# Optimization experiments

Hardware: AMD Instinct MI355X
Metric: run time of the kernel (lower is better)

The kernel has to match this reference:

```python
import jax, jax.numpy as jnp
import numpy as np

L, E, H, R = 6, 1024, 8, 33
DH = E // H
FF = 4 * E
B, S = 8, 512


def _layer_norm(x, g, b, eps=1e-5):
    m = jnp.mean(x, axis=-1, keepdims=True)
    v = jnp.mean(jnp.square(x - m), axis=-1, keepdims=True)
    return (x - m) * jax.lax.rsqrt(v + eps) * g + b


def setup_inputs() -> dict:
    key = jax.random.key(0)
    ks = jax.random.split(key, 24)
    rn = lambda k, shape, s=0.02: (jax.random.normal(k, shape, jnp.float32) * s)
    inp = {
        'enc_padded': jax.random.normal(ks[0], (B, S, E), jnp.float32),
        'relations': jax.random.randint(ks[1], (B, S, S), 0, R),
        'enc_lengths': jax.random.randint(ks[2], (B,), 1, S + 1),
        'Wq': rn(ks[3], (L, E, E)), 'bq': jnp.zeros((L, E), jnp.float32),
        'Wk': rn(ks[4], (L, E, E)), 'bk': jnp.zeros((L, E), jnp.float32),
        'Wv': rn(ks[5], (L, E, E)), 'bv': jnp.zeros((L, E), jnp.float32),
        'Wo': rn(ks[6], (L, E, E)), 'bo': jnp.zeros((L, E), jnp.float32),
        'rel_k': rn(ks[7], (L, R, DH)),
        'rel_v': rn(ks[8], (L, R, DH)),
        'W1': rn(ks[9], (L, E, FF)), 'b1': jnp.zeros((L, FF), jnp.float32),
        'W2': rn(ks[10], (L, FF, E)), 'b2': jnp.zeros((L, E), jnp.float32),
        'ln1_g': jnp.ones((L, E), jnp.float32), 'ln1_b': jnp.zeros((L, E), jnp.float32),
        'ln2_g': jnp.ones((L, E), jnp.float32), 'ln2_b': jnp.zeros((L, E), jnp.float32),
        'lnf_g': jnp.ones((E,), jnp.float32), 'lnf_b': jnp.zeros((E,), jnp.float32),
    }
    return inp


def reference(enc_padded, relations, enc_lengths, Wq, bq, Wk, bk, Wv, bv, Wo, bo,
              rel_k, rel_v, W1, b1, W2, b2, ln1_g, ln1_b, ln2_g, ln2_b, lnf_g, lnf_b):
    x = enc_padded  # [B,S,E]
    dt = x.dtype
    # attention mask: valid iff both query and key positions are within seq length
    pos = jnp.arange(S)
    valid = pos[None, :] < enc_lengths[:, None]            # [B,S]
    mask2d = valid[:, :, None] & valid[:, None, :]          # [B,S,S]
    # one-hot relation indicator, shared across layers (R=33 is small)
    rel_oh = jax.nn.one_hot(relations, R, dtype=dt)        # [B,S,S,R]
    scale = 1.0 / np.sqrt(DH).astype(np.float32)

    def split_heads(t):  # [B,S,E] -> [B,H,S,DH]
        return t.reshape(B, S, H, DH).transpose(0, 2, 1, 3)

    for l in range(L):
        # --- relation-aware self-attention (pre-LN sublayer) ---
        h = _layer_norm(x, ln1_g[l], ln1_b[l])
        q = split_heads(h @ Wq[l] + bq[l])
        k = split_heads(h @ Wk[l] + bk[l])
        v = split_heads(h @ Wv[l] + bv[l])
        scores = jnp.einsum('bhid,bhjd->bhij', q, k)
        # relation key bias: q_i . rel_k[rel[i,j]]  via small [B,H,S,R] GEMM + one-hot contraction
        qr = jnp.einsum('bhid,rd->bhir', q, rel_k[l])
        scores = (scores + jnp.einsum('bhir,bijr->bhij', qr, rel_oh)) * scale
        scores = jnp.where(mask2d[:, None], scores, jnp.asarray(-1e9, dt))
        attn = jax.nn.softmax(scores, axis=-1)              # [B,H,S,S]
        out = jnp.einsum('bhij,bhjd->bhid', attn, v)
        # relation value bias: sum_j attn_ij * rel_v[rel[i,j]]
        a_rel = jnp.einsum('bhij,bijr->bhir', attn, rel_oh)
        out = out + jnp.einsum('bhir,rd->bhid', a_rel, rel_v[l])
        out = out.transpose(0, 2, 1, 3).reshape(B, S, E) @ Wo[l] + bo[l]
        x = x + out
        # --- position-wise feed-forward (pre-LN sublayer) ---
        h2 = _layer_norm(x, ln2_g[l], ln2_b[l])
        x = x + (jax.nn.relu(h2 @ W1[l] + b1[l]) @ W2[l] + b2[l])
    return _layer_norm(x, lnf_g, lnf_b)
```

## Files before the change

### kernel.cpp

```cpp
#include <hip/hip_runtime.h>

#define LNUM 6
#define EDIM 1024
#define HNUM 8
#define DHD  128
#define RNUM 33
#define FFD  4096
#define BNUM 8
#define SLEN 512
#define TOK  (BNUM*SLEN)

typedef __attribute__((ext_vector_type(8))) short bf16x8;
typedef __attribute__((ext_vector_type(4))) float f32x4;
typedef unsigned short u16;
typedef unsigned int u32;

__device__ __forceinline__ u16 f2b(float f) {
  u32 u = __builtin_bit_cast(u32, f);
  u32 r = u + 0x7FFFu + ((u >> 16) & 1u);
  return (u16)(r >> 16);
}
__device__ __forceinline__ u32 pck(float a, float b) { return (u32)f2b(a) | ((u32)f2b(b) << 16); }

#define GL16(gp, lp) __builtin_amdgcn_global_load_lds(                        \
    (const __attribute__((address_space(1))) void*)(gp),                      \
    (__attribute__((address_space(3))) void*)(lp), 16, 0, 0)

#define WAITVM20 do { asm volatile("s_waitcnt vmcnt(20)" ::: "memory"); \
                      __builtin_amdgcn_sched_barrier(0); } while (0)
#define WAITVM16 do { asm volatile("s_waitcnt vmcnt(16)" ::: "memory"); \
                      __builtin_amdgcn_sched_barrier(0); } while (0)
#define WAITVM8 do { asm volatile("s_waitcnt vmcnt(8)" ::: "memory"); \
                     __builtin_amdgcn_sched_barrier(0); } while (0)
#define WAITVM0 do { asm volatile("s_waitcnt vmcnt(0)" ::: "memory"); \
                     __builtin_amdgcn_sched_barrier(0); } while (0)

template<int BF16OUT>
__global__ __launch_bounds__(256) void ln_kernel(const float* __restrict__ x,
                                                 const float* __restrict__ g,
                                                 const float* __restrict__ be,
                                                 void* __restrict__ o) {
  int row = blockIdx.x;
  int t = threadIdx.x;
  const float* xr = x + (size_t)row * EDIM;
  float4 xv = *reinterpret_cast<const float4*>(xr + t * 4);
  float s1 = xv.x + xv.y + xv.z + xv.w;
  float s2 = xv.x*xv.x + xv.y*xv.y + xv.z*xv.z + xv.w*xv.w;
#pragma unroll
  for (int off = 32; off >= 1; off >>= 1) {
    s1 += __shfl_down(s1, off, 64);
    s2 += __shfl_down(s2, off, 64);
  }
  __shared__ float r1[4], r2[4];
  if ((t & 63) == 0) { r1[t >> 6] = s1; r2[t >> 6] = s2; }
  __syncthreads();
  s1 = r1[0] + r1[1] + r1[2] + r1[3];
  s2 = r2[0] + r2[1] + r2[2] + r2[3];
  float mean = s1 * (1.0f / EDIM);
  float var  = s2 * (1.0f / EDIM) - mean * mean;
  float rstd = rsqrtf(var + 1e-5f);
  float4 gv = *reinterpret_cast<const float4*>(g + t * 4);
  float4 bv = *reinterpret_cast<const float4*>(be + t * 4);
  float o0 = (xv.x - mean) * rstd * gv.x + bv.x;
  float o1 = (xv.y - mean) * rstd * gv.y + bv.y;
  float o2 = (xv.z - mean) * rstd * gv.z + bv.z;
  float o3 = (xv.w - mean) * rstd * gv.w + bv.w;
  if (BF16OUT) {
    ushort4 ov; ov.x = f2b(o0); ov.y = f2b(o1); ov.z = f2b(o2); ov.w = f2b(o3);
    *reinterpret_cast<ushort4*>((u16*)o + (size_t)row * EDIM + t * 4) = ov;
  } else {
    *reinterpret_cast<float4*>((float*)o + (size_t)row * EDIM + t * 4) = make_float4(o0, o1, o2, o3);
  }
}

__global__ __launch_bounds__(256) void wtrans(const float* __restrict__ src0,
                                              u16* __restrict__ dst0,
                                              int Kd, int Nd, size_t sstride, size_t dstride) {
  __shared__ float Ts[32][33];
  const float* src = src0 + blockIdx.z * sstride;
  u16* dst = dst0 + blockIdx.z * dstride;
  int r0 = blockIdx.y * 32, c0 = blockIdx.x * 32;
  int ty = threadIdx.x >> 3, tx = threadIdx.x & 7;
  float4 v = *reinterpret_cast<const float4*>(src + (size_t)(r0 + ty) * Nd + c0 + tx * 4);
  Ts[ty][tx*4+0] = v.x; Ts[ty][tx*4+1] = v.y; Ts[ty][tx*4+2] = v.z; Ts[ty][tx*4+3] = v.w;
  __syncthreads();
  ushort4 o;
  o.x = f2b(Ts[tx*4+0][ty]); o.y = f2b(Ts[tx*4+1][ty]);
  o.z = f2b(Ts[tx*4+2][ty]); o.w = f2b(Ts[tx*4+3][ty]);
  *reinterpret_cast<ushort4*>(dst + (size_t)(c0 + ty) * Kd + r0 + tx * 4) = o;
}

__global__ __launch_bounds__(256) void relpack(const int* __restrict__ rel,
                                               unsigned char* __restrict__ out) {
  __shared__ int Ts[32][33];
  int bz = blockIdx.z;
  int r0 = blockIdx.y * 32, c0 = blockIdx.x * 32;
  int ty = threadIdx.x >> 3, tx = threadIdx.x & 7;
  const int* src = rel + (size_t)bz * SLEN * SLEN;
  int4 v = *reinterpret_cast<const int4*>(src + (size_t)(r0 + ty) * SLEN + c0 + tx * 4);
  Ts[ty][tx*4+0] = v.x; Ts[ty][tx*4+1] = v.y; Ts[ty][tx*4+2] = v.z; Ts[ty][tx*4+3] = v.w;
  __syncthreads();
  u32 o = (u32)(Ts[tx*4+0][ty] & 255) | ((u32)(Ts[tx*4+1][ty] & 255) << 8) |
          ((u32)(Ts[tx*4+2][ty] & 255) << 16) | ((u32)(Ts[tx*4+3][ty] & 255) << 24);
  *reinterpret_cast<u32*>(out + (size_t)bz * SLEN * SLEN + (size_t)(c0 + ty) * SLEN + r0 + tx * 4) = o;
}

template<int DEPTH, int BIASMODE, int ACT, int RES, int OUTBF16>
__global__ __launch_bounds__(256) void gemm_bt(const u16* __restrict__ A,
                                               const u16* __restrict__ B,
                                               const float* __restrict__ bias0,
                                               const float* __restrict__ bias1,
                                               const float* __restrict__ res,
                                               void* __restrict__ Cv,
                                               int M, int N, int K) {
  __shared__ u16 As[DEPTH][128 * 64];
  __shared__ u16 Bs[DEPTH][128 * 64];
  int t = threadIdx.x;
  int l = t & 63, w = t >> 6;
  int wm = w & 1, wn = w >> 1;
  int m0 = blockIdx.y * 128, n0 = blockIdx.x * 128;
  f32x4 acc[4][4] = {};
  const u16* Agp = A + (size_t)(m0 + w * 32 + (l >> 3)) * K + (l & 7) * 8;
  const u16* Bgp = B + (size_t)(n0 + w * 32 + (l >> 3)) * K + (l & 7) * 8;
  const int nst = K >> 6;
  auto issue = [&](int k0, int bi) {
#pragma unroll
    for (int u = 0; u < 4; ++u) {
      GL16(Agp + (size_t)(u * 8) * K + k0, &As[bi][w * 2048 + u * 512]);
      GL16(Bgp + (size_t)(u * 8) * K + k0, &Bs[bi][w * 2048 + u * 512]);
    }
  };
  issue(0, 0);
  if (DEPTH == 3 && nst > 1) issue(64, 1);
  for (int i = 0; i < nst; ++i) {
    int cur = (DEPTH == 3) ? (i % 3) : (i & 1);
    if (DEPTH == 3) {
      if (i + 2 < nst)      { issue((i + 2) * 64, (i + 2) % 3); WAITVM16; }
      else if (i + 1 < nst) { WAITVM8; }
      else                  { WAITVM0; }
    } else {
      if (i + 1 < nst) { issue((i + 1) * 64, cur ^ 1); WAITVM8; }
      else             { WAITVM0; }
    }
    __builtin_amdgcn_s_barrier();
    const u16* Asc = As[cur];
    const u16* Bsc = Bs[cur];
#pragma unroll
    for (int d4 = 0; d4 < 2; ++d4) {
      bf16x8 af[4];
#pragma unroll
      for (int fm = 0; fm < 4; ++fm) {
        int row = wm * 64 + fm * 16 + (l & 15);
        af[fm] = *reinterpret_cast<const bf16x8*>(Asc + row * 64 + (d4 * 4 + (l >> 4)) * 8);
      }
#pragma unroll
      for (int fn = 0; fn < 4; ++fn) {
        int row = wn * 64 + fn * 16 + (l & 15);
        bf16x8 bf = *reinterpret_cast<const bf16x8*>(Bsc + row * 64 + (d4 * 4 + (l >> 4)) * 8);
#pragma unroll
        for (int fm = 0; fm < 4; ++fm)
          acc[fm][fn] = __builtin_amdgcn_mfma_f32_16x16x32_bf16(af[fm], bf, acc[fm][fn], 0, 0, 0);
      }
    }
    __builtin_amdgcn_s_barrier();
  }
#pragma unroll
  for (int fm = 0; fm < 4; ++fm)
#pragma unroll
    for (int fn = 0; fn < 4; ++fn)
#pragma unroll
      for (int e = 0; e < 4; ++e) {
        int m = m0 + wm * 64 + fm * 16 + (l >> 4) * 4 + e;
        int n = n0 + wn * 64 + fn * 16 + (l & 15);
        float v = acc[fm][fn][e];
        if (BIASMODE == 0) v += bias0[n];
        if (BIASMODE == 1) v += bias0[m];
        if (BIASMODE == 2) v += (n < 1024) ? bias0[n] : bias1[n - 1024];
        if (ACT == 1) v = fmaxf(v, 0.f);
        if (RES == 1) v += res[(size_t)m * N + n];
        if (OUTBF16) ((u16*)Cv)[(size_t)m * N + n] = f2b(v);
        else ((float*)Cv)[(size_t)m * N + n] = v;
      }
}

template<int BIASMODE, int ACT, int RES, int OUTBF16>
__global__ __launch_bounds__(512, 2) void gemm_big(const u16* __restrict__ A,
                                                   const u16* __restrict__ B,
                                                   const float* __restrict__ bias0,
                                                   const float* __restrict__ res,
                                                   void* __restrict__ Cv,
                                                   int M, int N, int K) {
  __shared__ u16 As[2][256 * 64];
  __shared__ u16 Bs[2][256 * 64];
  int t = threadIdx.x;
  int l = t & 63, w = t >> 6;
  int wm = w >> 2, wn = w & 3;
  int m0 = blockIdx.y * 256, n0 = blockIdx.x * 256;
  f32x4 acc[8][4] = {};
  const u16* Agp = A + (size_t)(m0 + w * 32 + (l >> 3)) * K + (l & 7) * 8;
  const u16* Bgp = B + (size_t)(n0 + w * 32 + (l >> 3)) * K + (l & 7) * 8;
  const int nst = K >> 6;
  auto issue = [&](int k0, int bi) {
#pragma unroll
    for (int u = 0; u < 4; ++u) {
      GL16(Agp + (size_t)(u * 8) * K + k0, &As[bi][w * 2048 + u * 512]);
      GL16(Bgp + (size_t)(u * 8) * K + k0, &Bs[bi][w * 2048 + u * 512]);
    }
  };
  issue(0, 0);
  for (int i = 0; i < nst; ++i) {
    int cur = i & 1;
    if (i + 1 < nst) { issue((i + 1) * 64, cur ^ 1); WAITVM8; }
    else             { WAITVM0; }
    __builtin_amdgcn_s_barrier();
    const u16* Asc = As[cur];
    const u16* Bsc = Bs[cur];
#pragma unroll
    for (int d4 = 0; d4 < 2; ++d4) {
      bf16x8 bf[4];
#pragma unroll
      for (int fn = 0; fn < 4; ++fn) {
        int row = wn * 64 + fn * 16 + (l & 15);
        bf[fn] = *reinterpret_cast<const bf16x8*>(Bsc + row * 64 + (d4 * 4 + (l >> 4)) * 8);
      }
#pragma unroll
      for (int fm = 0; fm < 8; ++fm) {
        int row = wm * 128 + fm * 16 + (l & 15);
        bf16x8 af = *reinterpret_cast<const bf16x8*>(Asc + row * 64 + (d4 * 4 + (l >> 4)) * 8);
#pragma unroll
        for (int fn = 0; fn < 4; ++fn)
          acc[fm][fn] = __builtin_amdgcn_mfma_f32_16x16x32_bf16(af, bf[fn], acc[fm][fn], 0, 0, 0);
      }
    }
    __builtin_amdgcn_s_barrier();
  }
#pragma unroll
  for (int fm = 0; fm < 8; ++fm)
#pragma unroll
    for (int fn = 0; fn < 4; ++fn)
#pragma unroll
      for (int e = 0; e < 4; ++e) {
        int m = m0 + wm * 128 + fm * 16 + (l >> 4) * 4 + e;
        int n = n0 + wn * 64 + fn * 16 + (l & 15);
        float v = acc[fm][fn][e];
        if (BIASMODE == 0) v += bias0[n];
        if (ACT == 1) v = fmaxf(v, 0.f);
        if (RES == 1) v += res[(size_t)m * N + n];
        if (OUTBF16) ((u16*)Cv)[(size_t)m * N + n] = f2b(v);
        else ((float*)Cv)[(size_t)m * N + n] = v;
      }
}

#define A_P  0
#define A_Q  16384
#define A_PS 32768
#define A_QR 40960
#define A_AR 50176
#define A_LS 59392
#define A_SM 59648

__global__ __launch_bounds__(256, 2) void attn_kernel(const u16* __restrict__ qk,
                                                      const u16* __restrict__ vt,
                                                      const unsigned char* __restrict__ rel8,
                                                      const int* __restrict__ lens,
                                                      const float* __restrict__ relk,
                                                      const float* __restrict__ relv,
                                                      u16* __restrict__ outb) {
  __align__(16) __shared__ char sm[A_SM];
  char*  Pb  = sm + A_P;
  char*  Qb  = sm + A_Q;
  char*  PSb = sm + A_PS;
  float* QR  = (float*)(sm + A_QR);
  float* AREL = (float*)(sm + A_AR);
  float* LSUM = (float*)(sm + A_LS);

  const int t = threadIdx.x;
  const int l = t & 63, w = t >> 6;
  const int lg = l >> 4;
  const int ll = l & 15;
  const int bx = blockIdx.x;
  const int xcd = bx & 7, rem = bx >> 3, slot = rem & 7, it = rem >> 3;
  const int g = slot * 8 + xcd;
  const int b = g >> 3, hh = g & 7;
  const int i0 = it * 64;
  const int len = lens[b];
  const float scale = 0.08838834764831845f;
  char* PSw = PSb + w * 2048;

  auto issueK = [&](int kt) {
#pragma unroll
    for (int u = 0; u < 4; ++u) {
      int row = w * 16 + u * 4 + (lg);
      int sb = (ll * 16) ^ (((u * 4 + lg) & 7) << 4);
      const u16* gp = qk + (size_t)(b * SLEN + kt * 64 + row) * 2048 + 1024 + hh * DHD + (sb >> 1);
      GL16(gp, Pb + (w * 4 + u) * 1024);
    }
  };
  auto issueV = [&](int kt) {
#pragma unroll
    for (int u = 0; u < 4; ++u) {
      int row = w * 32 + u * 8 + (l >> 3);
      int sb = ((l & 7) * 16) ^ ((l >> 3) << 4);
      const u16* gp = vt + (size_t)(hh * DHD + row) * TOK + b * SLEN + kt * 64 + (sb >> 1);
      GL16(gp, Qb + (w * 4 + u) * 1024);
    }
  };
  const unsigned char* relbase = rel8 + (size_t)b * SLEN * SLEN + (i0 + w * 16 + lg * 4);

  for (int idx = l; idx < 16 * 36; idx += 64) AREL[w * 16 * 36 + idx] = 0.f;
  if (t < 192) {
    int r = t >> 2, sub = t & 3;
#pragma unroll
    for (int u = 0; u < 4; ++u) {
      int seg = sub * 4 + u;
      uint4 o;
      if (r < RNUM) {
        float4 f0 = *reinterpret_cast<const float4*>(relk + r * DHD + seg * 8);
        float4 f1 = *reinterpret_cast<const float4*>(relk + r * DHD + seg * 8 + 4);
        o.x = pck(f0.x, f0.y); o.y = pck(f0.z, f0.w);
        o.z = pck(f1.x, f1.y); o.w = pck(f1.z, f1.w);
      } else { o.x = o.y = o.z = o.w = 0u; }
      *reinterpret_cast<uint4*>(Pb + r * 256 + ((seg * 16) ^ ((r & 7) << 4))) = o;
    }
  }
  bf16x8 aq[4];
  {
    const u16* qrow = qk + (size_t)(b * SLEN + i0 + w * 16 + ll) * 2048 + hh * DHD;
#pragma unroll
    for (int d4 = 0; d4 < 4; ++d4)
      aq[d4] = *reinterpret_cast<const bf16x8*>(qrow + (d4 * 4 + lg) * 8);
  }
  __syncthreads();
#pragma unroll
  for (int rb = 0; rb < 3; ++rb) {
    f32x4 acc = {};
#pragma unroll
    for (int d4 = 0; d4 < 4; ++d4) {
      int rr = rb * 16 + ll;
      bf16x8 br = *reinterpret_cast<const bf16x8*>(Pb + rr * 256 + (((d4 * 4 + lg) * 16) ^ ((rr & 7) << 4)));
      acc = __builtin_amdgcn_mfma_f32_16x16x32_bf16(aq[d4], br, acc, 0, 0, 0);
    }
    int col = rb * 16 + ll;
    if (col < 36)
#pragma unroll
      for (int e = 0; e < 4; ++e)
        QR[(w * 16 + lg * 4 + e) * 36 + col] = acc[e];
  }
  __syncthreads();
  issueK(0);
  u32 relw[4];
  {
    const unsigned char* rb = relbase + (size_t)ll * SLEN;
#pragma unroll
    for (int fj = 0; fj < 4; ++fj)
      relw[fj] = *reinterpret_cast<const u32*>(rb + (size_t)(fj * 16) * SLEN);
  }

  bool rowv[4];
#pragma unroll
  for (int e = 0; e < 4; ++e) rowv[e] = (i0 + w * 16 + lg * 4 + e) < len;

  float m_[4];
#pragma unroll
  for (int e = 0; e < 4; ++e) m_[e] = -3.0e38f;
  f32x4 oacc[8] = {};

  for (int kt = 0; kt < 8; ++kt) {
    issueV(kt);
    WAITVM20;
    __builtin_amdgcn_s_barrier();
    __builtin_amdgcn_s_setprio(1);
    f32x4 sacc[4];
#pragma unroll
    for (int fj = 0; fj < 4; ++fj) {
      f32x4 a = {};
#pragma unroll
      for (int d4 = 0; d4 < 4; ++d4) {
        int row = fj * 16 + ll;
        bf16x8 bk_ = *reinterpret_cast<const bf16x8*>(Pb + row * 256 + (((d4 * 4 + lg) * 16) ^ ((row & 7) << 4)));
        a = __builtin_amdgcn_mfma_f32_16x16x32_bf16(aq[d4], bk_, a, 0, 0, 0);
      }
      sacc[fj] = a;
    }
    __builtin_amdgcn_s_setprio(0);
#pragma unroll
    for (int fj = 0; fj < 4; ++fj) {
      bool colv = (kt * 64 + fj * 16 + ll) < len;
      u32 rw = relw[fj];
#pragma unroll
      for (int e = 0; e < 4; ++e) {
        int r = (rw >> (8 * e)) & 255;
        float s = (sacc[fj][e] + QR[(w * 16 + lg * 4 + e) * 36 + r]) * scale;
        s = (rowv[e] && colv) ? s : -1e9f;
        sacc[fj][e] = s;
      }
    }
    float pl[4];
#pragma unroll
    for (int e = 0; e < 4; ++e)
      pl[e] = fmaxf(fmaxf(sacc[0][e], sacc[1][e]), fmaxf(sacc[2][e], sacc[3][e]));
    bool ok = (pl[0] <= m_[0] + 8.f) && (pl[1] <= m_[1] + 8.f) &&
              (pl[2] <= m_[2] + 8.f) && (pl[3] <= m_[3] + 8.f);
    if (!__all(ok)) {
#pragma unroll
      for (int e = 0; e < 4; ++e) {
        float px = pl[e];
        px = fmaxf(px, __shfl_xor(px, 1, 64));
        px = fmaxf(px, __shfl_xor(px, 2, 64));
        px = fmaxf(px, __shfl_xor(px, 4, 64));
        px = fmaxf(px, __shfl_xor(px, 8, 64));
        float mn = fmaxf(m_[e], px);
        float f = __expf(m_[e] - mn);
        m_[e] = mn;
#pragma unroll
        for (int fd = 0; fd < 8; ++fd) oacc[fd][e] *= f;
        if (f != 1.0f) {
          int row = w * 16 + lg * 4 + e;
          AREL[row * 36 + ll] *= f;
          AREL[row * 36 + 16 + ll] *= f;
          if (ll == 0) AREL[row * 36 + 32] *= f;
        }
      }
    }
#pragma unroll
    for (int fj = 0; fj < 4; ++fj) {
      u32 rw = relw[fj];
#pragma unroll
      for (int e = 0; e < 4; ++e) {
        float p = __expf(sacc[fj][e] - m_[e]);
        int iloc = lg * 4 + e;
        atomicAdd(&AREL[(w * 16 + iloc) * 36 + ((rw >> (8 * e)) & 255)], p);
        *reinterpret_cast<u16*>(PSw + iloc * 128 + (((fj * 16 + ll) * 2) ^ ((iloc & 7) << 4))) = f2b(p);
      }
    }
    __builtin_amdgcn_s_barrier();
    if (kt < 7) {
      issueK(kt + 1);
      {
        const unsigned char* rb = relbase + (size_t)((kt + 1) * 64 + ll) * SLEN;
#pragma unroll
        for (int fj = 0; fj < 4; ++fj)
          relw[fj] = *reinterpret_cast<const u32*>(rb + (size_t)(fj * 16) * SLEN);
      }
      WAITVM20;
    } else {
      WAITVM0;
    }
    __builtin_amdgcn_s_barrier();
    __builtin_amdgcn_s_setprio(1);
#pragma unroll
    for (int kc = 0; kc < 2; ++kc) {
      bf16x8 pa = *reinterpret_cast<const bf16x8*>(PSw + ll * 128 + (((kc * 4 + lg) * 16) ^ ((ll & 7) << 4)));
#pragma unroll
      for (int fd = 0; fd < 8; ++fd) {
        int row = fd * 16 + ll;
        bf16x8 vb = *reinterpret_cast<const bf16x8*>(Qb + row * 128 + (((kc * 4 + lg) * 16) ^ ((row & 7) << 4)));
        oacc[fd] = __builtin_amdgcn_mfma_f32_16x16x32_bf16(pa, vb, oacc[fd], 0, 0, 0);
      }
    }
    __builtin_amdgcn_s_setprio(0);
    __builtin_amdgcn_s_barrier();
  }
  if (l < 16) {
    int row = w * 16 + l;
    float s = 0.f;
    for (int r = 0; r < RNUM; ++r) s += AREL[row * 36 + r];
    LSUM[row] = s;
  }
#pragma unroll
  for (int e = 0; e < 4; ++e) {
    float inv = 1.0f / LSUM[w * 16 + lg * 4 + e];
#pragma unroll
    for (int fd = 0; fd < 8; ++fd) oacc[fd][e] *= inv;
  }
  for (int idx = t; idx < 128 * 64; idx += 256) {
    int d = idx >> 6, r = idx & 63;
    u16 v = (r < RNUM) ? f2b(relv[r * DHD + d]) : (u16)0;
    *reinterpret_cast<u16*>(Pb + d * 128 + ((r * 2) ^ ((d & 7) << 4))) = v;
  }
  for (int idx = l; idx < 1024; idx += 64) {
    int ri = idx >> 6, r = idx & 63;
    int row = w * 16 + ri;
    float v = (r < RNUM) ? AREL[row * 36 + r] * (1.0f / LSUM[row]) : 0.f;
    *reinterpret_cast<u16*>(PSw + ri * 128 + ((r * 2) ^ ((ri & 7) << 4))) = f2b(v);
  }
  __syncthreads();
#pragma unroll
  for (int kc = 0; kc < 2; ++kc) {
    bf16x8 pa = *reinterpret_cast<const bf16x8*>(PSw + ll * 128 + (((kc * 4 + lg) * 16) ^ ((ll & 7) << 4)));
#pragma unroll
    for (int fd = 0; fd < 8; ++fd) {
      int row = fd * 16 + ll;
      bf16x8 vb = *reinterpret_cast<const bf16x8*>(Pb + row * 128 + (((kc * 4 + lg) * 16) ^ ((row & 7) << 4)));
      oacc[fd] = __builtin_amdgcn_mfma_f32_16x16x32_bf16(pa, vb, oacc[fd], 0, 0, 0);
    }
  }
  char* OSw = Qb + w * 4096;
#pragma unroll
  for (int fd = 0; fd < 8; ++fd)
#pragma unroll
    for (int e = 0; e < 4; ++e)
      *reinterpret_cast<u16*>(OSw + ((lg * 4 + e) * 128 + fd * 16 + ll) * 2) = f2b(oacc[fd][e]);
  __syncthreads();
  {
    int ri = l >> 2, q4 = l & 3;
    const char* srcb = OSw + ri * 256 + q4 * 64;
    u16* dst = outb + (size_t)(b * SLEN + i0 + w * 16 + ri) * EDIM + hh * DHD + q4 * 32;
    uint4 x0 = *reinterpret_cast<const uint4*>(srcb);
    uint4 x1 = *reinterpret_cast<const uint4*>(srcb + 16);
    uint4 x2 = *reinterpret_cast<const uint4*>(srcb + 32);
    uint4 x3 = *reinterpret_cast<const uint4*>(srcb + 48);
    *reinterpret_cast<uint4*>(dst)      = x0;
    *reinterpret_cast<uint4*>(dst + 8)  = x1;
    *reinterpret_cast<uint4*>(dst + 16) = x2;
    *reinterpret_cast<uint4*>(dst + 24) = x3;
  }
}

extern "C" void kernel_launch(void* const* d_in, const int* in_sizes, int n_in,
                              void* d_out, int out_size, void* d_ws, size_t ws_size,
                              hipStream_t stream) {
  const float* enc  = (const float*)d_in[0];
  const int*   rel  = (const int*)d_in[1];
  const int*   lens = (const int*)d_in[2];
  const float* Wq = (const float*)d_in[3];
  const float* bq = (const float*)d_in[4];
  const float* Wk = (const float*)d_in[5];
  const float* bk = (const float*)d_in[6];
  const float* Wv = (const float*)d_in[7];
  const float* bv = (const float*)d_in[8];
  const float* Wo = (const float*)d_in[9];
  const float* bo = (const float*)d_in[10];
  const float* relk = (const float*)d_in[11];
  const float* relv = (const float*)d_in[12];
  const float* W1 = (const float*)d_in[13];
  const float* b1 = (const float*)d_in[14];
  const float* W2 = (const float*)d_in[15];
  const float* b2 = (const float*)d_in[16];
  const float* ln1g = (const float*)d_in[17];
  const float* ln1b = (const float*)d_in[18];
  const float* ln2g = (const float*)d_in[19];
  const float* ln2b = (const float*)d_in[20];
  const float* lnfg = (const float*)d_in[21];
  const float* lnfb = (const float*)d_in[22];
  float* out = (float*)d_out;

  char* W = (char*)d_ws;
  u16* h     = (u16*)W;
  unsigned char* rel8_h = (unsigned char*)W;
  char* U    = W + 8388608;
  u16* qkb   = (u16*)U;
  u16* vtb   = (u16*)(U + 16777216);
  u16* attno = (u16*)(U + 25165824);
  u16* mid   = (u16*)U;
  bool xin = ws_size >= (size_t)83886080;
  float* x = xin ? (float*)(W + 41943040) : out;
  size_t wt_off = xin ? 58720256 : 41943040;
  char* WT = W + wt_off;
  bool big = ws_size >= (size_t)209715200;

  const size_t EE = (size_t)EDIM * EDIM;
  const size_t EF = (size_t)EDIM * FFD;
  size_t wt_bytes = (big ? 6 : 1) * (size_t)(2*EE + EE + EE + EF + EF) * 2;
  bool rel_ded = ws_size >= wt_off + wt_bytes + (size_t)BNUM * SLEN * SLEN + 256;
  unsigned char* rel8 = rel_ded ? (unsigned char*)(WT + wt_bytes) : rel8_h;

  u16 *WqkT, *WvT, *WoT, *W1T, *W2T;
  dim3 blk(256);
  if (big) {
    u16* wqk_all = (u16*)WT;
    u16* wv_all  = wqk_all + 6 * 2 * EE;
    u16* wo_all  = wv_all + 6 * EE;
    u16* w1_all  = wo_all + 6 * EE;
    u16* w2_all  = w1_all + 6 * EF;
    wtrans<<<dim3(32, 32, 6), blk, 0, stream>>>(Wq, wqk_all, 1024, 1024, EE, 2 * EE);
    wtrans<<<dim3(32, 32, 6), blk, 0, stream>>>(Wk, wqk_all + EE, 1024, 1024, EE, 2 * EE);
    wtrans<<<dim3(32, 32, 6), blk, 0, stream>>>(Wv, wv_all, 1024, 1024, EE, EE);
    wtrans<<<dim3(32, 32, 6), blk, 0, stream>>>(Wo, wo_all, 1024, 1024, EE, EE);
    wtrans<<<dim3(128, 32, 6), blk, 0, stream>>>(W1, w1_all, 1024, 4096, EF, EF);
    wtrans<<<dim3(32, 128, 6), blk, 0, stream>>>(W2, w2_all, 4096, 1024, EF, EF);
    WqkT = wqk_all; WvT = wv_all; WoT = wo_all; W1T = w1_all; W2T = w2_all;
  } else {
    WqkT = (u16*)WT;
    WvT  = WqkT + 2 * EE;
    WoT  = WvT + EE;
    W1T  = WoT + EE;
    W2T  = W1T + EF;
  }
  if (rel_ded) relpack<<<dim3(16, 16, 8), blk, 0, stream>>>(rel, rel8);

  dim3 gLN(TOK);
  for (int ll = 0; ll < LNUM; ++ll) {
    u16 *wqkT, *wvT, *woT, *w1T, *w2T;
    if (big) {
      wqkT = WqkT + (size_t)ll * 2 * EE; wvT = WvT + (size_t)ll * EE; woT = WoT + (size_t)ll * EE;
      w1T = W1T + (size_t)ll * EF; w2T = W2T + (size_t)ll * EF;
    } else {
      wqkT = WqkT; wvT = WvT; woT = WoT; w1T = W1T; w2T = W2T;
      wtrans<<<dim3(32, 32, 1), blk, 0, stream>>>(Wq + ll * EE, wqkT, 1024, 1024, 0, 0);
      wtrans<<<dim3(32, 32, 1), blk, 0, stream>>>(Wk + ll * EE, wqkT + EE, 1024, 1024, 0, 0);
      wtrans<<<dim3(32, 32, 1), blk, 0, stream>>>(Wv + ll * EE, wvT, 1024, 1024, 0, 0);
      wtrans<<<dim3(32, 32, 1), blk, 0, stream>>>(Wo + ll * EE, woT, 1024, 1024, 0, 0);
      wtrans<<<dim3(128, 32, 1), blk, 0, stream>>>(W1 + ll * EF, w1T, 1024, 4096, 0, 0);
      wtrans<<<dim3(32, 128, 1), blk, 0, stream>>>(W2 + ll * EF, w2T, 4096, 1024, 0, 0);
    }
    const float* xin_p = (ll == 0) ? enc : x;
    ln_kernel<1><<<gLN, blk, 0, stream>>>(xin_p, ln1g + ll * EDIM, ln1b + ll * EDIM, h);
    gemm_bt<2, 2, 0, 0, 1><<<dim3(16, 32), blk, 0, stream>>>(h, wqkT, bq + ll * EDIM, bk + ll * EDIM,
                                                             nullptr, qkb, TOK, 2048, EDIM);
    gemm_bt<3, 1, 0, 0, 1><<<dim3(32, 8), blk, 0, stream>>>(wvT, h, bv + ll * EDIM, nullptr,
                                                            nullptr, vtb, EDIM, TOK, EDIM);
    if (!rel_ded) relpack<<<dim3(16, 16, 8), blk, 0, stream>>>(rel, rel8);
    attn_kernel<<<dim3(512), blk, 0, stream>>>(qkb, vtb, rel8, lens,
                                               relk + (size_t)ll * RNUM * DHD,
                                               relv + (size_t)ll * RNUM * DHD, attno);
    gemm_bt<3, 0, 0, 1, 0><<<dim3(8, 32), blk, 0, stream>>>(attno, woT, bo + ll * EDIM, nullptr,
                                                            xin_p, x, TOK, EDIM, EDIM);
    ln_kernel<1><<<gLN, blk, 0, stream>>>(x, ln2g + ll * EDIM, ln2b + ll * EDIM, h);
    gemm_big<0, 1, 0, 1><<<dim3(FFD / 256, TOK / 256), dim3(512), 0, stream>>>(
        h, w1T, b1 + ll * FFD, nullptr, mid, TOK, FFD, EDIM);
    gemm_bt<3, 0, 0, 1, 0><<<dim3(8, 32), blk, 0, stream>>>(mid, w2T, b2 + ll * EDIM, nullptr,
                                                            x, x, TOK, EDIM, FFD);
  }
  ln_kernel<0><<<gLN, blk, 0, stream>>>(x, lnfg, lnfb, out);
}
```

Before: 2.158 ms.

## Halve attention KV tile and shrink LDS to fit four blocks per CU

```diff
diff --git a/kernel.cpp b/kernel.cpp
--- a/kernel.cpp
+++ b/kernel.cpp
@@ -20,17 +20,20 @@
   u32 r = u + 0x7FFFu + ((u >> 16) & 1u);
   return (u16)(r >> 16);
 }
+__device__ __forceinline__ float b2f(u16 v) {
+  return __builtin_bit_cast(float, ((u32)v) << 16);
+}
 __device__ __forceinline__ u32 pck(float a, float b) { return (u32)f2b(a) | ((u32)f2b(b) << 16); }
 
 #define GL16(gp, lp) __builtin_amdgcn_global_load_lds(                        \
     (const __attribute__((address_space(1))) void*)(gp),                      \
     (__attribute__((address_space(3))) void*)(lp), 16, 0, 0)
 
-#define WAITVM20 do { asm volatile("s_waitcnt vmcnt(20)" ::: "memory"); \
-                      __builtin_amdgcn_sched_barrier(0); } while (0)
 #define WAITVM16 do { asm volatile("s_waitcnt vmcnt(16)" ::: "memory"); \
                       __builtin_amdgcn_sched_barrier(0); } while (0)
 #define WAITVM8 do { asm volatile("s_waitcnt vmcnt(8)" ::: "memory"); \
+                     __builtin_amdgcn_sched_barrier(0); } while (0)
+#define WAITVM4 do { asm volatile("s_waitcnt vmcnt(4)" ::: "memory"); \
                      __builtin_amdgcn_sched_barrier(0); } while (0)
 #define WAITVM0 do { asm volatile("s_waitcnt vmcnt(0)" ::: "memory"); \
                      __builtin_amdgcn_sched_barrier(0); } while (0)
@@ -252,14 +255,14 @@
 }
 
 #define A_P  0
-#define A_Q  16384
-#define A_PS 32768
-#define A_QR 40960
-#define A_AR 50176
-#define A_LS 59392
-#define A_SM 59648
-
-__global__ __launch_bounds__(256, 2) void attn_kernel(const u16* __restrict__ qk,
+#define A_Q  8192
+#define A_PS 16384
+#define A_QR 24576
+#define A_AR 29184
+#define A_LS 38400
+#define A_SM 38656
+
+__global__ __launch_bounds__(256, 4) void attn_kernel(const u16* __restrict__ qk,
                                                       const u16* __restrict__ vt,
                                                       const unsigned char* __restrict__ rel8,
                                                       const int* __restrict__ lens,
@@ -270,7 +273,7 @@
   char*  Pb  = sm + A_P;
   char*  Qb  = sm + A_Q;
   char*  PSb = sm + A_PS;
-  float* QR  = (float*)(sm + A_QR);
+  u16*   QRb = (u16*)(sm + A_QR);
   float* AREL = (float*)(sm + A_AR);
   float* LSUM = (float*)(sm + A_LS);
 
@@ -289,20 +292,22 @@
 
   auto issueK = [&](int kt) {
 #pragma unroll
-    for (int u = 0; u < 4; ++u) {
-      int row = w * 16 + u * 4 + (lg);
-      int sb = (ll * 16) ^ (((u * 4 + lg) & 7) << 4);
-      const u16* gp = qk + (size_t)(b * SLEN + kt * 64 + row) * 2048 + 1024 + hh * DHD + (sb >> 1);
-      GL16(gp, Pb + (w * 4 + u) * 1024);
+    for (int u = 0; u < 2; ++u) {
+      int c = w * 2 + u;
+      int row = c * 4 + lg;
+      int sb = (ll * 16) ^ ((row & 7) << 4);
+      const u16* gp = qk + (size_t)(b * SLEN + kt * 32 + row) * 2048 + 1024 + hh * DHD + (sb >> 1);
+      GL16(gp, Pb + c * 1024);
     }
   };
   auto issueV = [&](int kt) {
 #pragma unroll
-    for (int u = 0; u < 4; ++u) {
-      int row = w * 32 + u * 8 + (l >> 3);
-      int sb = ((l & 7) * 16) ^ ((l >> 3) << 4);
-      const u16* gp = vt + (size_t)(hh * DHD + row) * TOK + b * SLEN + kt * 64 + (sb >> 1);
-      GL16(gp, Qb + (w * 4 + u) * 1024);
+    for (int u = 0; u < 2; ++u) {
+      int c = w * 2 + u;
+      int row = c * 16 + (l >> 2);
+      int sb = ((l & 3) * 16) ^ (((l >> 2) & 3) << 4);
+      const u16* gp = vt + (size_t)(hh * DHD + row) * TOK + b * SLEN + kt * 32 + (sb >> 1);
+      GL16(gp, Qb + c * 1024);
     }
   };
   const unsigned char* relbase = rel8 + (size_t)b * SLEN * SLEN + (i0 + w * 16 + lg * 4);
@@ -344,15 +349,15 @@
     if (col < 36)
 #pragma unroll
       for (int e = 0; e < 4; ++e)
-        QR[(w * 16 + lg * 4 + e) * 36 + col] = acc[e];
+        QRb[(w * 16 + lg * 4 + e) * 36 + col] = f2b(acc[e]);
   }
   __syncthreads();
   issueK(0);
-  u32 relw[4];
+  u32 relw[2];
   {
     const unsigned char* rb = relbase + (size_t)ll * SLEN;
 #pragma unroll
-    for (int fj = 0; fj < 4; ++fj)
+    for (int fj = 0; fj < 2; ++fj)
       relw[fj] = *reinterpret_cast<const u32*>(rb + (size_t)(fj * 16) * SLEN);
   }
 
@@ -365,14 +370,14 @@
   for (int e = 0; e < 4; ++e) m_[e] = -3.0e38f;
   f32x4 oacc[8] = {};
 
-  for (int kt = 0; kt < 8; ++kt) {
+  for (int kt = 0; kt < 16; ++kt) {
     issueV(kt);
-    WAITVM20;
+    WAITVM4;
     __builtin_amdgcn_s_barrier();
     __builtin_amdgcn_s_setprio(1);
-    f32x4 sacc[4];
-#pragma unroll
-    for (int fj = 0; fj < 4; ++fj) {
+    f32x4 sacc[2];
+#pragma unroll
+    for (int fj = 0; fj < 2; ++fj) {
       f32x4 a = {};
 #pragma unroll
       for (int d4 = 0; d4 < 4; ++d4) {
@@ -384,13 +389,13 @@
     }
     __builtin_amdgcn_s_setprio(0);
 #pragma unroll
-    for (int fj = 0; fj < 4; ++fj) {
-      bool colv = (kt * 64 + fj * 16 + ll) < len;
+    for (int fj = 0; fj < 2; ++fj) {
+      bool colv = (kt * 32 + fj * 16 + ll) < len;
       u32 rw = relw[fj];
 #pragma unroll
       for (int e = 0; e < 4; ++e) {
         int r = (rw >> (8 * e)) & 255;
-        float s = (sacc[fj][e] + QR[(w * 16 + lg * 4 + e) * 36 + r]) * scale;
+        float s = (sacc[fj][e] + b2f(QRb[(w * 16 + lg * 4 + e) * 36 + r])) * scale;
         s = (rowv[e] && colv) ? s : -1e9f;
         sacc[fj][e] = s;
       }
@@ -398,7 +403,7 @@
     float pl[4];
 #pragma unroll
     for (int e = 0; e < 4; ++e)
-      pl[e] = fmaxf(fmaxf(sacc[0][e], sacc[1][e]), fmaxf(sacc[2][e], sacc[3][e]));
+      pl[e] = fmaxf(sacc[0][e], sacc[1][e]);
     bool ok = (pl[0] <= m_[0] + 8.f) && (pl[1] <= m_[1] + 8.f) &&
               (pl[2] <= m_[2] + 8.f) && (pl[3] <= m_[3] + 8.f);
     if (!__all(ok)) {
@@ -423,38 +428,37 @@
       }
     }
 #pragma unroll
-    for (int fj = 0; fj < 4; ++fj) {
+    for (int fj = 0; fj < 2; ++fj) {
       u32 rw = relw[fj];
 #pragma unroll
       for (int e = 0; e < 4; ++e) {
         float p = __expf(sacc[fj][e] - m_[e]);
         int iloc = lg * 4 + e;
         atomicAdd(&AREL[(w * 16 + iloc) * 36 + ((rw >> (8 * e)) & 255)], p);
-        *reinterpret_cast<u16*>(PSw + iloc * 128 + (((fj * 16 + ll) * 2) ^ ((iloc & 7) << 4))) = f2b(p);
-      }
-    }
-    __builtin_amdgcn_s_barrier();
-    if (kt < 7) {
+        *reinterpret_cast<u16*>(PSw + iloc * 64 + (((fj * 16 + ll) * 2) ^ ((iloc & 3) << 4))) = f2b(p);
+      }
+    }
+    __builtin_amdgcn_s_barrier();
+    if (kt < 15) {
       issueK(kt + 1);
       {
-        const unsigned char* rb = relbase + (size_t)((kt + 1) * 64 + ll) * SLEN;
-#pragma unroll
-        for (int fj = 0; fj < 4; ++fj)
+        const unsigned char* rb = relbase + (size_t)((kt + 1) * 32 + ll) * SLEN;
+#pragma unroll
+        for (int fj = 0; fj < 2; ++fj)
           relw[fj] = *reinterpret_cast<const u32*>(rb + (size_t)(fj * 16) * SLEN);
       }
-      WAITVM20;
+      WAITVM4;
     } else {
       WAITVM0;
     }
     __builtin_amdgcn_s_barrier();
     __builtin_amdgcn_s_setprio(1);
-#pragma unroll
-    for (int kc = 0; kc < 2; ++kc) {
-      bf16x8 pa = *reinterpret_cast<const bf16x8*>(PSw + ll * 128 + (((kc * 4 + lg) * 16) ^ ((ll & 7) << 4)));
+    {
+      bf16x8 pa = *reinterpret_cast<const bf16x8*>(PSw + ll * 64 + ((lg * 16) ^ ((ll & 3) << 4)));
 #pragma unroll
       for (int fd = 0; fd < 8; ++fd) {
         int row = fd * 16 + ll;
-        bf16x8 vb = *reinterpret_cast<const bf16x8*>(Qb + row * 128 + (((kc * 4 + lg) * 16) ^ ((row & 7) << 4)));
+        bf16x8 vb = *reinterpret_cast<const bf16x8*>(Qb + row * 64 + ((lg * 16) ^ ((row & 3) << 4)));
         oacc[fd] = __builtin_amdgcn_mfma_f32_16x16x32_bf16(pa, vb, oacc[fd], 0, 0, 0);
       }
     }
@@ -495,7 +499,8 @@
       oacc[fd] = __builtin_amdgcn_mfma_f32_16x16x32_bf16(pa, vb, oacc[fd], 0, 0, 0);
     }
   }
-  char* OSw = Qb + w * 4096;
+  __syncthreads();
+  char* OSw = Pb + w * 4096;
 #pragma unroll
   for (int fd = 0; fd < 8; ++fd)
 #pragma unroll
```

Result: slower. 2.206 ms (+2.2%).
